# Kernel tuning notes

Hardware: AMD Instinct MI355X
Metric: run time of the kernel (lower is better)

## Reference

```python
import jax, jax.numpy as jnp
import numpy as np

NUM_CLASSES = 80
STRIDES = (8, 16, 32)
FEAT_HW = ((80, 80), (40, 40), (20, 20))
B = 32
MAX_GT = 60


def setup_inputs() -> dict:
    key = jax.random.key(0)
    ks = jax.random.split(key, 6)
    feats = {}
    for i, (s, (h, w)) in enumerate(zip(STRIDES, FEAT_HW)):
        feats[f"feat{s}"] = jax.random.normal(ks[i], (B, 5 + NUM_CLASSES, h, w), jnp.float32)
    u = jax.random.uniform(ks[3], (B, MAX_GT, 4), jnp.float32)
    # cx,cy in [0,640), w,h in [8,128): realistic pixel-space gt boxes for a 640x640 image
    gt_boxes = jnp.concatenate([u[..., :2] * 640.0, u[..., 2:] * 120.0 + 8.0], -1)
    gt_classes = jax.random.randint(ks[4], (B, MAX_GT), 0, NUM_CLASSES)
    num_gts = jax.random.randint(ks[5], (B,), 1, MAX_GT + 1)
    return dict(feat8=feats["feat8"], feat16=feats["feat16"], feat32=feats["feat32"],
                gt_boxes=gt_boxes, gt_classes=gt_classes, num_gts=num_gts)


def _decode(feat, stride):
    # torch get_output_and_grid: xy=(raw+grid)*stride, wh=exp(raw)*stride
    b, c, h, w = feat.shape
    yv, xv = jnp.meshgrid(jnp.arange(h), jnp.arange(w), indexing="ij")
    gx = xv.reshape(-1).astype(feat.dtype)  # [H*W]
    gy = yv.reshape(-1).astype(feat.dtype)
    out = feat.reshape(b, c, h * w).transpose(0, 2, 1)  # [B,A,C]
    xy = (out[..., :2] + jnp.stack([gx, gy], -1)[None]) * stride
    wh = jnp.exp(out[..., 2:4]) * stride
    return jnp.concatenate([xy, wh, out[..., 4:]], -1), gx, gy


def _pair_iou(a, b):
    # a: [G,4] xywh, b: [A,4] xywh -> [G,A] IoU (bboxes_iou, xyxy=False)
    tl = jnp.maximum(a[:, None, :2] - a[:, None, 2:] * 0.5, b[None, :, :2] - b[None, :, 2:] * 0.5)
    br = jnp.minimum(a[:, None, :2] + a[:, None, 2:] * 0.5, b[None, :, :2] + b[None, :, 2:] * 0.5)
    en = jnp.all(tl < br, -1)
    inter = jnp.where(en, jnp.prod(br - tl, -1), 0.0)
    area_a = jnp.prod(a[:, 2:], -1)
    area_b = jnp.prod(b[:, 2:], -1)
    return inter / (area_a[:, None] + area_b[None, :] - inter + 1e-16)


def _bce_logits(x, t):
    return jnp.maximum(x, 0.0) - x * t + jnp.log1p(jnp.exp(-jnp.abs(x)))


def _iou_loss(pred, tgt):
    # IOUloss(loss_type='iou'): 1 - iou^2, per box
    tl = jnp.maximum(pred[..., :2] - pred[..., 2:] * 0.5, tgt[..., :2] - tgt[..., 2:] * 0.5)
    br = jnp.minimum(pred[..., :2] + pred[..., 2:] * 0.5, tgt[..., :2] + tgt[..., 2:] * 0.5)
    en = jnp.all(tl < br, -1)
    inter = jnp.where(en, jnp.prod(br - tl, -1), 0.0)
    union = jnp.prod(pred[..., 2:], -1) + jnp.prod(tgt[..., 2:], -1) - inter
    iou = inter / (union + 1e-16)
    return 1.0 - iou ** 2


def _assign(boxes, cls_lo, obj_lo, gtb, gtc, vmask, cx, cy, st):
    # SimOTA per image. boxes [A,4], cls_lo [A,C], obj_lo [A], gtb [G,4], gtc [G] int,
    # vmask [G] bool (gt padding), cx/cy/st [A] anchor centers & strides.
    G, A = gtb.shape[0], boxes.shape[0]
    iou = _pair_iou(gtb, boxes)  # [G,A]
    gx, gy = gtb[:, :1], gtb[:, 1:2]
    gw, gh = gtb[:, 2:3], gtb[:, 3:4]
    in_box = ((cx[None] > gx - 0.5 * gw) & (cx[None] < gx + 0.5 * gw) &
              (cy[None] > gy - 0.5 * gh) & (cy[None] < gy + 0.5 * gh))
    R = 2.5  # center sampling radius (in strides)
    in_ctr = ((cx[None] > gx - R * st[None]) & (cx[None] < gx + R * st[None]) &
              (cy[None] > gy - R * st[None]) & (cy[None] < gy + R * st[None]))
    fg = ((in_box | in_ctr) & vmask[:, None]).any(0)  # [A] candidate anchors
    in_both = (in_box & in_ctr).astype(boxes.dtype)
    # pairwise cls cost: BCE(sqrt(sig(cls)*sig(obj)), onehot(gt_cls)).sum(-1),
    # decomposed to avoid the [G,A,C] tensor: sum_c bce0 + (bce1-bce0)[gt_cls]
    p = jnp.clip(jnp.sqrt(jax.nn.sigmoid(cls_lo) * jax.nn.sigmoid(obj_lo)[:, None]), 1e-7, 1.0 - 1e-7)
    bce1 = -jnp.log(p)          # [A,C]
    bce0 = -jnp.log(1.0 - p)    # [A,C]
    cls_cost = bce0.sum(-1)[None, :] + (bce1 - bce0)[:, gtc].T  # [G,A]
    cost = (cls_cost + 3.0 * (-jnp.log(iou + 1e-8))
            + 100000.0 * (1.0 - in_both)
            + 1e9 * (~fg)[None, :].astype(boxes.dtype)
            + 1e9 * (~vmask)[:, None].astype(boxes.dtype))
    K = 10  # n_candidate_k
    topk_ious, _ = jax.lax.top_k(iou * fg[None, :], K)
    dyn_k = jnp.maximum(topk_ious.sum(-1).astype(jnp.int32), 1)  # clamp(int(sum), min=1)
    _, pos = jax.lax.top_k(-cost, K)  # [G,K] lowest-cost anchors per gt
    sel = (jnp.arange(K)[None, :] < dyn_k[:, None]).astype(boxes.dtype)
    matching = jnp.zeros((G, A), boxes.dtype).at[jnp.arange(G)[:, None], pos].set(sel)
    matching = matching * vmask[:, None].astype(boxes.dtype)
    # resolve anchors claimed by >1 gt: keep min-cost gt
    conflict = matching.sum(0) > 1
    best_gt = jnp.argmin(cost, axis=0)  # [A]
    matching = jnp.where(conflict[None, :], jax.nn.one_hot(best_gt, G, dtype=matching.dtype).T, matching)
    fg_final = matching.sum(0) > 0  # [A]
    matched = jnp.argmax(matching, axis=0)  # [A]
    pred_iou = (matching * iou).sum(0)  # [A]
    cls_t = jax.nn.one_hot(gtc[matched], NUM_CLASSES, dtype=boxes.dtype) * pred_iou[:, None]
    reg_t = gtb[matched]
    return fg_final, cls_t, reg_t


def _forward(feat8, feat16, feat32, gt_boxes, gt_classes, num_gts):
    outs, cxs, cys, sts = [], [], [], []
    for f, s in zip((feat8, feat16, feat32), STRIDES):
        o, gx, gy = _decode(f, float(s))
        outs.append(o)
        cxs.append((gx + 0.5) * s)
        cys.append((gy + 0.5) * s)
        sts.append(jnp.full_like(gx, s))
    preds = jnp.concatenate(outs, 1)  # [B,A,5+C]
    cx = jnp.concatenate(cxs)
    cy = jnp.concatenate(cys)
    st = jnp.concatenate(sts)
    boxes = preds[..., :4]
    obj_lo = preds[..., 4]
    cls_lo = preds[..., 5:]
    vmask = jnp.arange(MAX_GT)[None, :] < num_gts[:, None]
    fg, cls_t, reg_t = jax.vmap(_assign, in_axes=(0, 0, 0, 0, 0, 0, None, None, None))(
        boxes, cls_lo, obj_lo, gt_boxes, gt_classes, vmask, cx, cy, st)
    # SimOTA assignment is no_grad in YOLOX: targets are constants wrt preds
    fg = jax.lax.stop_gradient(fg)
    cls_t = jax.lax.stop_gradient(cls_t)
    reg_t = jax.lax.stop_gradient(reg_t)
    fg_f = fg.astype(boxes.dtype)
    num_fg = jnp.maximum(fg_f.sum(), 1.0)
    loss_iou = (_iou_loss(boxes, reg_t) * fg_f).sum()
    loss_obj = _bce_logits(obj_lo, fg_f * 0.9).sum()  # obj_targets * 0.9 smoothing
    loss_cls = (_bce_logits(cls_lo, cls_t) * fg_f[..., None]).sum()
    REG_WEIGHT = 5.0
    return (REG_WEIGHT * loss_iou + loss_obj + loss_cls) / num_fg


def reference(feat8, feat16, feat32, gt_boxes, gt_classes, num_gts):
    return _forward(feat8, feat16, feat32, gt_boxes, gt_classes, num_gts)
```

## Files before the change

kernel.cpp:

```cpp
#include <hip/hip_runtime.h>

constexpr int kB = 32;
constexpr int kA = 8400;
constexpr int kG = 60;
constexpr int kC = 80;
constexpr int kK = 10;
constexpr int kNBx = (kA + 255)/256;
constexpr int kNB = kNBx * kB;

__device__ __forceinline__ float fexp(float x){ return __expf(x); }
__device__ __forceinline__ float flog(float x){ return __logf(x); }
__device__ __forceinline__ float frcp(float x){ return __builtin_amdgcn_rcpf(x); }
__device__ __forceinline__ float frsq(float x){ return __builtin_amdgcn_rsqf(x); }
__device__ __forceinline__ float fsqrt(float x){ return __builtin_amdgcn_sqrtf(x); }
__device__ __forceinline__ float fdiv(float a, float b){ return a * __builtin_amdgcn_rcpf(b); }
__device__ __forceinline__ float sigm(float x){ return frcp(1.0f + fexp(-x)); }
__device__ __forceinline__ float bce(float x, float t){
  return fmaxf(x, 0.0f) - x*t + flog(1.0f + fexp(-fabsf(x)));
}

__device__ __forceinline__ unsigned ordbits(float v){
  unsigned u = __float_as_uint(v);
  return (u & 0x80000000u) ? ~u : (u | 0x80000000u);
}
__device__ __forceinline__ float unpackf(unsigned k){
  return __uint_as_float((k & 0x80000000u) ? (k & 0x7fffffffu) : ~k);
}

struct AInfo { int x, y; float st; };
__device__ __forceinline__ AInfo ainfo(int a){
  AInfo r;
  if (a < 6400)      { r.x = a % 80;           r.y = a / 80;           r.st = 8.0f;  }
  else if (a < 8000) { int l = a-6400; r.x = l % 40; r.y = l / 40;     r.st = 16.0f; }
  else               { int l = a-8000; r.x = l % 20; r.y = l / 20;     r.st = 32.0f; }
  return r;
}

__device__ __forceinline__ float featv(const float* __restrict__ f8,
                                       const float* __restrict__ f16,
                                       const float* __restrict__ f32x,
                                       int b, int ch, int a){
  if (a < 6400) return f8 [(b*85 + ch)*6400 + a];
  if (a < 8000) return f16[(b*85 + ch)*1600 + (a - 6400)];
  return             f32x[(b*85 + ch)*400  + (a - 8000)];
}

__device__ __forceinline__ float pair_iou(float4 g, float4 p){
  float tlx = fmaxf(g.x - g.z*0.5f, p.x - p.z*0.5f);
  float tly = fmaxf(g.y - g.w*0.5f, p.y - p.w*0.5f);
  float brx = fminf(g.x + g.z*0.5f, p.x + p.z*0.5f);
  float bry = fminf(g.y + g.w*0.5f, p.y + p.w*0.5f);
  float inter = (tlx < brx && tly < bry) ? (brx-tlx)*(bry-tly) : 0.0f;
  return fdiv(inter, g.z*g.w + p.z*p.w - inter + 1e-16f);
}

__device__ __forceinline__ float cost_core(float iou, float cl, float obs, float b0sum,
                                           int a, float4 gt, int fg_a){
  AInfo ai = ainfo(a);
  float cx = ((float)ai.x + 0.5f)*ai.st;
  float cy = ((float)ai.y + 0.5f)*ai.st;
  bool in_box = (cx > gt.x - 0.5f*gt.z) && (cx < gt.x + 0.5f*gt.z)
             && (cy > gt.y - 0.5f*gt.w) && (cy < gt.y + 0.5f*gt.w);
  bool in_ctr = (cx > gt.x - 2.5f*ai.st) && (cx < gt.x + 2.5f*ai.st)
             && (cy > gt.y - 2.5f*ai.st) && (cy < gt.y + 2.5f*ai.st);
  float p = fsqrt(sigm(cl) * obs);
  p = fminf(fmaxf(p, 1e-7f), 1.0f - 1e-7f);
  float diff = -flog(p) + flog(1.0f - p);
  float c = b0sum + diff;
  c += 3.0f * (-flog(iou + 1e-8f));
  c += (in_box && in_ctr) ? 0.0f : 100000.0f;
  c += fg_a ? 0.0f : 1000000000.0f;
  return c;
}

__device__ __forceinline__ unsigned long long wave_max64(unsigned long long v){
  #pragma unroll
  for (int off = 32; off; off >>= 1){
    unsigned long long o = __shfl_xor(v, off, 64);
    if (o > v) v = o;
  }
  return v;
}

__global__ __launch_bounds__(256, 4) void k_decode(
    const float* __restrict__ f8, const float* __restrict__ f16, const float* __restrict__ f32x,
    const float* __restrict__ gtb, const int* __restrict__ ngts,
    float* __restrict__ boxes, float* __restrict__ boxesZ,
    float* __restrict__ objl, float* __restrict__ b0s,
    float* __restrict__ bceS, float* __restrict__ obsA,
    int* __restrict__ fg, int* __restrict__ cnt, int* __restrict__ mtch){
  int b = blockIdx.y;
  int tid = threadIdx.x;
  int a = blockIdx.x*256 + tid;
  __shared__ float4 sg[kG];
  if (tid < kG) sg[tid] = ((const float4*)gtb)[b*kG + tid];
  __syncthreads();
  if (a >= kA) return;
  int ng = ngts[b];
  const float* base; int hw, off; float st_; int gx, gy;
  if (a < 6400)      { base=f8;   hw=6400; off=a;        st_=8.0f;  gx=off%80; gy=off/80; }
  else if (a < 8000) { base=f16;  hw=1600; off=a-6400;   st_=16.0f; gx=off%40; gy=off/40; }
  else               { base=f32x; hw=400;  off=a-8000;   st_=32.0f; gx=off%20; gy=off/20; }
  const float* p0 = base + ((size_t)b*85)*hw + off;
  const float* pc = p0 + (size_t)5*hw;
  float t0 = p0[0];
  float t1 = p0[(size_t)hw];
  float t2 = p0[(size_t)2*hw];
  float t3 = p0[(size_t)3*hw];
  float ob = p0[(size_t)4*hw];
  float cl[kC];
  #pragma unroll
  for (int j = 0; j < kC; ++j) cl[j] = pc[(size_t)j*hw];
  __builtin_amdgcn_sched_barrier(0);
  float4 bx;
  bx.x = (t0 + (float)gx) * st_;
  bx.y = (t1 + (float)gy) * st_;
  bx.z = fexp(t2) * st_;
  bx.w = fexp(t3) * st_;
  int idx = b*kA + a;
  ((float4*)boxes)[idx] = bx;
  objl[idx] = ob;
  float obs = sigm(ob);
  obsA[idx] = obs;
  cnt[idx] = 0;
  mtch[idx] = 0x7fffffff;
  float cx = ((float)gx + 0.5f)*st_;
  float cy = ((float)gy + 0.5f)*st_;
  int f = 0;
  for (int g = 0; g < ng; ++g){
    float4 gt = sg[g];
    bool in_box = (cx > gt.x - 0.5f*gt.z) && (cx < gt.x + 0.5f*gt.z)
               && (cy > gt.y - 0.5f*gt.w) && (cy < gt.y + 0.5f*gt.w);
    bool in_ctr = (cx > gt.x - 2.5f*st_) && (cx < gt.x + 2.5f*st_)
               && (cy > gt.y - 2.5f*st_) && (cy < gt.y + 2.5f*st_);
    if (in_box || in_ctr){ f = 1; break; }
  }
  fg[idx] = f;
  ((float4*)boxesZ)[idx] = f ? bx : make_float4(0.0f,0.0f,0.0f,0.0f);
  float so = fsqrt(obs);
  float s = 0.0f;
  float sumCl = 0.0f;
  float slogv = 0.0f;
  #pragma unroll
  for (int grp = 0; grp < kC/8; ++grp){
    float prodS = 1.0f, prodV = 1.0f;
    #pragma unroll
    for (int j = 0; j < 8; ++j){
      float c = cl[grp*8 + j];
      float u = fexp(-c);
      float v = 1.0f + u;
      float p = so * frsq(v);
      p = fminf(fmaxf(p, 1e-7f), 1.0f - 1e-7f);
      prodS *= (1.0f - p);
      prodV *= v;
      sumCl += c;
    }
    s -= flog(prodS);
    slogv += flog(prodV);
  }
  b0s[idx] = s;
  bceS[idx] = sumCl + slogv;
}

__global__ __launch_bounds__(256) void k_assign(
    const float* __restrict__ f8, const float* __restrict__ f16, const float* __restrict__ f32x,
    const float* __restrict__ gtb, const int* __restrict__ gtc, const int* __restrict__ ngts,
    const float* __restrict__ boxes, const float* __restrict__ boxesZ,
    const float* __restrict__ obsA, const float* __restrict__ b0s,
    const int* __restrict__ fg,
    int* __restrict__ cnt, int* __restrict__ mtch){
  int b = blockIdx.x / kG;
  int g = blockIdx.x % kG;
  if (g >= ngts[b]) return;
  int tid = threadIdx.x;
  int lane = tid & 63, wid = tid >> 6;
  float4 gt = ((const float4*)gtb)[b*kG + g];
  int cls = gtc[b*kG + g];
  const float4* bx4 = (const float4*)boxes;
  const float4* bz4 = (const float4*)boxesZ;
  const float* c8  = f8   + ((size_t)b*85 + 5 + cls)*6400;
  const float* c16 = f16  + ((size_t)b*85 + 5 + cls)*1600;
  const float* c32 = f32x + ((size_t)b*85 + 5 + cls)*400;

  __shared__ unsigned long long lds_k[4*kK];
  __shared__ int lds_cnt[4];
  __shared__ int s_dynk;

  unsigned long long k1[kK];
  #pragma unroll
  for (int i = 0; i < kK; ++i) k1[i] = 0ull;

  for (int i = tid; i < kA; i += 256){
    float4 bx = bz4[b*kA + i];
    float v = pair_iou(gt, bx);
    unsigned long long key1 = ((unsigned long long)ordbits(v) << 32) | (unsigned)(~i);
    if (key1 > k1[kK-1]){
      k1[kK-1] = key1;
      #pragma unroll
      for (int i2 = kK-1; i2 > 0; --i2)
        if (k1[i2] > k1[i2-1]){ unsigned long long t = k1[i2]; k1[i2] = k1[i2-1]; k1[i2-1] = t; }
    }
  }
  {
    unsigned long long wtop = 0ull;
    #pragma unroll
    for (int k = 0; k < kK; ++k){
      unsigned long long best = wave_max64(k1[0]);
      if (k1[0] == best){
        #pragma unroll
        for (int i2 = 0; i2 < kK-1; ++i2) k1[i2] = k1[i2+1];
        k1[kK-1] = 0ull;
      }
      if (lane == k) wtop = best;
    }
    if (lane < kK) lds_k[wid*kK + lane] = wtop;
  }
  __syncthreads();
  if (wid == 0){
    unsigned long long key = (lane < 4*kK) ? lds_k[lane] : 0ull;
    float ksum = 0.0f;
    #pragma unroll
    for (int k = 0; k < kK; ++k){
      unsigned long long best = wave_max64(key);
      if (key == best) key = 0ull;
      if (best) ksum += unpackf((unsigned)(best >> 32));
    }
    if (lane == 0) s_dynk = max((int)ksum, 1);
  }
  __syncthreads();
  int dynk = s_dynk;

  int x00,y00,nx0,n0, x01,y01,nx1,n1, x02,y02,nx2,n2;
  {
    auto rect = [&](float st, int W, int& rx0, int& ry0, int& rnx, int& rn){
      float lox = fmaxf(gt.x - 0.5f*gt.z, gt.x - 2.5f*st);
      float hix = fminf(gt.x + 0.5f*gt.z, gt.x + 2.5f*st);
      float loy = fmaxf(gt.y - 0.5f*gt.w, gt.y - 2.5f*st);
      float hiy = fminf(gt.y + 0.5f*gt.w, gt.y + 2.5f*st);
      float rs = frcp(st);
      int ax0 = max(0,   (int)floorf(lox*rs - 0.5f) - 1);
      int ax1 = min(W-1, (int)ceilf (hix*rs - 0.5f) + 1);
      int ay0 = max(0,   (int)floorf(loy*rs - 0.5f) - 1);
      int ay1 = min(W-1, (int)ceilf (hiy*rs - 0.5f) + 1);
      rx0 = ax0; ry0 = ay0;
      rnx = max(0, ax1 - ax0 + 1);
      int rny = max(0, ay1 - ay0 + 1);
      rn = rnx * rny;
    };
    rect( 8.0f, 80, x00, y00, nx0, n0);
    rect(16.0f, 40, x01, y01, nx1, n1);
    rect(32.0f, 20, x02, y02, nx2, n2);
  }
  int total = n0 + n1 + n2;

  unsigned long long ck = 0ull;
  int nvalid = 0;
  if (tid < total){
    int i = tid, ix, iy, a; float st;
    if (i < n0)           { ix = x00 + i % nx0; iy = y00 + i / nx0; a = iy*80 + ix;          st = 8.0f;  }
    else if (i < n0 + n1) { int j = i - n0;      ix = x01 + j % nx1; iy = y01 + j / nx1; a = 6400 + iy*40 + ix; st = 16.0f; }
    else                  { int j = i - n0 - n1; ix = x02 + j % nx2; iy = y02 + j / nx2; a = 8000 + iy*20 + ix; st = 32.0f; }
    float cx = ((float)ix + 0.5f)*st;
    float cy = ((float)iy + 0.5f)*st;
    bool in_box = (cx > gt.x - 0.5f*gt.z) && (cx < gt.x + 0.5f*gt.z)
               && (cy > gt.y - 0.5f*gt.w) && (cy < gt.y + 0.5f*gt.w);
    bool in_ctr = (cx > gt.x - 2.5f*st) && (cx < gt.x + 2.5f*st)
               && (cy > gt.y - 2.5f*st) && (cy < gt.y + 2.5f*st);
    if (in_box && in_ctr){
      int idx = b*kA + a;
      float4 bx = bx4[idx];
      float iou = pair_iou(gt, bx);
      float cl = (a < 6400) ? c8[a] : (a < 8000) ? c16[a-6400] : c32[a-8000];
      float c = cost_core(iou, cl, obsA[idx], b0s[idx], a, gt, 1);
      ck = ~(((unsigned long long)ordbits(c) << 32) | (unsigned)a);
      nvalid = 1;
    }
  }
  {
    unsigned long long bal = __ballot(nvalid);
    if (lane == 0) lds_cnt[wid] = __popcll(bal);
    unsigned long long wtop = 0ull;
    #pragma unroll
    for (int k = 0; k < kK; ++k){
      unsigned long long best = wave_max64(ck);
      if (ck == best) ck = 0ull;
      if (lane == k) wtop = best;
    }
    if (lane < kK) lds_k[wid*kK + lane] = wtop;
  }
  __syncthreads();
  int cnt_total = lds_cnt[0] + lds_cnt[1] + lds_cnt[2] + lds_cnt[3];
  bool fb = (dynk > cnt_total);

  if (!fb){
    if (wid == 0){
      unsigned long long key = (lane < 4*kK) ? lds_k[lane] : 0ull;
      unsigned long long mine = 0ull;
      #pragma unroll
      for (int k = 0; k < kK; ++k){
        unsigned long long best = wave_max64(key);
        if (key == best) key = 0ull;
        if (lane == k) mine = best;
      }
      if (lane < dynk && mine){
        int a = (int)((unsigned)(~mine));
        atomicAdd(&cnt[b*kA + a], 1);
        atomicMin(&mtch[b*kA + a], g);
      }
    }
    return;
  }

  __syncthreads();
  unsigned long long k2[kK];
  #pragma unroll
  for (int i = 0; i < kK; ++i) k2[i] = 0ull;
  for (int i = tid; i < kA; i += 256){
    int idx = b*kA + i;
    float4 bx = bx4[idx];
    float iou = pair_iou(gt, bx);
    int fga = fg[idx];
    float cl = (i < 6400) ? c8[i] : (i < 8000) ? c16[i-6400] : c32[i-8000];
    float c = cost_core(iou, cl, obsA[idx], b0s[idx], i, gt, fga);
    unsigned long long key2 = ~(((unsigned long long)ordbits(c) << 32) | (unsigned)i);
    if (key2 > k2[kK-1]){
      k2[kK-1] = key2;
      #pragma unroll
      for (int i2 = kK-1; i2 > 0; --i2)
        if (k2[i2] > k2[i2-1]){ unsigned long long t = k2[i2]; k2[i2] = k2[i2-1]; k2[i2-1] = t; }
    }
  }
  {
    unsigned long long wtop = 0ull;
    #pragma unroll
    for (int k = 0; k < kK; ++k){
      unsigned long long best = wave_max64(k2[0]);
      if (k2[0] == best){
        #pragma unroll
        for (int i2 = 0; i2 < kK-1; ++i2) k2[i2] = k2[i2+1];
        k2[kK-1] = 0ull;
      }
      if (lane == k) wtop = best;
    }
    if (lane < kK) lds_k[wid*kK + lane] = wtop;
  }
  __syncthreads();
  if (wid == 0){
    unsigned long long key = (lane < 4*kK) ? lds_k[lane] : 0ull;
    unsigned long long mine = 0ull;
    #pragma unroll
    for (int k = 0; k < kK; ++k){
      unsigned long long best = wave_max64(key);
      if (key == best) key = 0ull;
      if (lane == k) mine = best;
    }
    if (lane < dynk && mine){
      int a = (int)((unsigned)(~mine));
      atomicAdd(&cnt[b*kA + a], 1);
      atomicMin(&mtch[b*kA + a], g);
    }
  }
}

__global__ __launch_bounds__(256) void k_loss(
    const float* __restrict__ f8, const float* __restrict__ f16, const float* __restrict__ f32x,
    const float* __restrict__ gtb, const int* __restrict__ gtc, const int* __restrict__ ngts,
    const float* __restrict__ boxes, const float* __restrict__ objl, const float* __restrict__ b0s,
    const float* __restrict__ bceS, const float* __restrict__ obsA,
    const int* __restrict__ fg, const int* __restrict__ cnt, const int* __restrict__ mtch,
    float4* __restrict__ pacc){
  int b = blockIdx.y;
  int a = blockIdx.x*256 + threadIdx.x;
  int tid = threadIdx.x;
  __shared__ float4 sg[kG];
  __shared__ int scls[kG];
  if (tid < kG){ sg[tid] = ((const float4*)gtb)[b*kG + tid]; scls[tid] = gtc[b*kG + tid]; }
  __syncthreads();
  float li = 0.0f, lo = 0.0f, lc = 0.0f, nf = 0.0f;
  bool valid = (a < kA);
  int idx = valid ? (b*kA + a) : (b*kA);
  int c = valid ? cnt[idx] : 0;
  float ob = valid ? objl[idx] : 0.0f;
  float4 bx = valid ? ((const float4*)boxes)[idx] : make_float4(0,0,1,1);

  float fgf = 0.0f; int mg = 0;
  if (valid && c == 1){ mg = mtch[idx]; fgf = 1.0f; }
  bool need = valid && (c > 1);
  if (__any(need)){
    if (need){
      int ng = ngts[b];
      float b0 = b0s[idx];
      float obs = obsA[idx];
      int fga = fg[idx];
      float bestc = 3.0e38f; int bg = 0;
      for (int g = 0; g < ng; ++g){
        float iou = pair_iou(sg[g], bx);
        float cl = featv(f8,f16,f32x,b,5+scls[g],a);
        float cst = cost_core(iou, cl, obs, b0, a, sg[g], fga);
        if (cst < bestc){ bestc = cst; bg = g; }
      }
      mg = bg; fgf = 1.0f;
    }
  }
  if (valid){
    lo = bce(ob, fgf*0.9f);
    if (fgf > 0.0f){
      nf = 1.0f;
      float4 r = sg[mg];
      float piou = pair_iou(r, bx);
      float tlx = fmaxf(bx.x - bx.z*0.5f, r.x - r.z*0.5f);
      float tly = fmaxf(bx.y - bx.w*0.5f, r.y - r.w*0.5f);
      float brx = fminf(bx.x + bx.z*0.5f, r.x + r.z*0.5f);
      float bry = fminf(bx.y + bx.w*0.5f, r.y + r.w*0.5f);
      float inter = (tlx < brx && tly < bry) ? (brx-tlx)*(bry-tly) : 0.0f;
      float un = bx.z*bx.w + r.z*r.w - inter;
      float iou = fdiv(inter, un + 1e-16f);
      li = 1.0f - iou*iou;
      int tc = scls[mg];
      float cl_tc = featv(f8,f16,f32x,b,5+tc,a);
      lc = bceS[idx] - piou * cl_tc;
    }
  }
  for (int off = 32; off > 0; off >>= 1){
    li += __shfl_down(li, off, 64);
    lo += __shfl_down(lo, off, 64);
    lc += __shfl_down(lc, off, 64);
    nf += __shfl_down(nf, off, 64);
  }
  __shared__ float4 wred[4];
  int wid = tid >> 6;
  if ((tid & 63) == 0) wred[wid] = make_float4(li, lo, lc, nf);
  __syncthreads();
  if (tid == 0){
    float4 t = wred[0];
    for (int w = 1; w < 4; ++w){
      float4 o = wred[w];
      t.x += o.x; t.y += o.y; t.z += o.z; t.w += o.w;
    }
    pacc[blockIdx.y * gridDim.x + blockIdx.x] = t;
  }
}

__global__ __launch_bounds__(256) void k_final(
    const float4* __restrict__ pacc, float* __restrict__ out){
  int tid = threadIdx.x;
  float li = 0.0f, lo = 0.0f, lc = 0.0f, nf = 0.0f;
  for (int i = tid; i < kNB; i += 256){
    float4 p = pacc[i];
    li += p.x; lo += p.y; lc += p.z; nf += p.w;
  }
  for (int off = 32; off > 0; off >>= 1){
    li += __shfl_down(li, off, 64);
    lo += __shfl_down(lo, off, 64);
    lc += __shfl_down(lc, off, 64);
    nf += __shfl_down(nf, off, 64);
  }
  __shared__ float4 wred[4];
  int wid = tid >> 6;
  if ((tid & 63) == 0) wred[wid] = make_float4(li, lo, lc, nf);
  __syncthreads();
  if (tid == 0){
    float4 t = wred[0];
    for (int w = 1; w < 4; ++w){
      float4 o = wred[w];
      t.x += o.x; t.y += o.y; t.z += o.z; t.w += o.w;
    }
    out[0] = (5.0f*t.x + t.y + t.z) * frcp(fmaxf(t.w, 1.0f));
  }
}

extern "C" void kernel_launch(void* const* d_in, const int* in_sizes, int n_in,
                              void* d_out, int out_size, void* d_ws, size_t ws_size,
                              hipStream_t stream) {
  (void)in_sizes; (void)n_in; (void)out_size; (void)ws_size;
  const float* f8   = (const float*)d_in[0];
  const float* f16  = (const float*)d_in[1];
  const float* f32x = (const float*)d_in[2];
  const float* gtb  = (const float*)d_in[3];
  const int*   gtc  = (const int*)d_in[4];
  const int*   ngts = (const int*)d_in[5];
  float* out = (float*)d_out;

  const size_t BA = (size_t)kB*kA;
  float* ws     = (float*)d_ws;
  float* boxes  = ws;
  float* boxesZ = boxes  + BA*4;
  float* objl   = boxesZ + BA*4;
  float* b0s    = objl   + BA;
  float* bceS   = b0s    + BA;
  float* obsA   = bceS   + BA;
  int*   fg     = (int*)(obsA + BA);
  int*   cnt    = fg  + BA;
  int*   mtch   = cnt + BA;
  float4* pacc  = (float4*)(mtch + BA);

  dim3 gBA(kNBx, kB);
  k_decode<<<gBA, dim3(256), 0, stream>>>(f8,f16,f32x,gtb,ngts,boxes,boxesZ,objl,b0s,bceS,obsA,fg,cnt,mtch);
  k_assign<<<dim3(kB*kG), dim3(256), 0, stream>>>(f8,f16,f32x,gtb,gtc,ngts,boxes,boxesZ,obsA,b0s,fg,cnt,mtch);
  k_loss<<<gBA, dim3(256), 0, stream>>>(f8,f16,f32x,gtb,gtc,ngts,boxes,objl,b0s,bceS,obsA,fg,cnt,mtch,pacc);
  k_final<<<dim3(1), dim3(256), 0, stream>>>(pacc, out);
}
```

Before: 203.4 us.

## Split decode class work across half-waves and fuse final reduction into loss kernel

The decode kernel now assigns two lanes per anchor, with each half-wave handling a different subset of the 80 class channels. The partial log-sums are combined through cross-lane shuffles, which raises parallelism and lowers per-thread register pressure (the 80-float class array is gone). The final reduction kernel is removed. The last loss block, detected with an atomic counter and threadfence, now does the global sum, which saves one launch. This adds a memset launch and an atomic last-block pattern, and the half-wave split is uneven (4 vs 6 groups).

```diff
diff --git a/kernel.cpp b/kernel.cpp
--- a/kernel.cpp
+++ b/kernel.cpp
@@ -7,6 +7,7 @@
 constexpr int kK = 10;
 constexpr int kNBx = (kA + 255)/256;
 constexpr int kNB = kNBx * kB;
+constexpr int kNDx = (kA + 127)/128;
 
 __device__ __forceinline__ float fexp(float x){ return __expf(x); }
 __device__ __forceinline__ float flog(float x){ return __logf(x); }
@@ -82,7 +83,7 @@
   return v;
 }
 
-__global__ __launch_bounds__(256, 4) void k_decode(
+__global__ __launch_bounds__(256) void k_decode(
     const float* __restrict__ f8, const float* __restrict__ f16, const float* __restrict__ f32x,
     const float* __restrict__ gtb, const int* __restrict__ ngts,
     float* __restrict__ boxes, float* __restrict__ boxesZ,
@@ -91,7 +92,10 @@
     int* __restrict__ fg, int* __restrict__ cnt, int* __restrict__ mtch){
   int b = blockIdx.y;
   int tid = threadIdx.x;
-  int a = blockIdx.x*256 + tid;
+  int wid = tid >> 6, lane = tid & 63;
+  int half = lane >> 5;
+  int l32 = lane & 31;
+  int a = blockIdx.x*128 + wid*32 + l32;
   __shared__ float4 sg[kG];
   if (tid < kG) sg[tid] = ((const float4*)gtb)[b*kG + tid];
   __syncthreads();
@@ -103,63 +107,85 @@
   else               { base=f32x; hw=400;  off=a-8000;   st_=32.0f; gx=off%20; gy=off/20; }
   const float* p0 = base + ((size_t)b*85)*hw + off;
   const float* pc = p0 + (size_t)5*hw;
-  float t0 = p0[0];
-  float t1 = p0[(size_t)hw];
-  float t2 = p0[(size_t)2*hw];
-  float t3 = p0[(size_t)3*hw];
+  int idx = b*kA + a;
+
   float ob = p0[(size_t)4*hw];
-  float cl[kC];
+  float obs = sigm(ob);
+  float so = fsqrt(obs);
+
+  int gbase = half ? 4 : 0;
+  int ngrp  = half ? 6 : 4;
+  float lS[6], lV[6];
+  float scl = 0.0f;
   #pragma unroll
-  for (int j = 0; j < kC; ++j) cl[j] = pc[(size_t)j*hw];
-  __builtin_amdgcn_sched_barrier(0);
-  float4 bx;
-  bx.x = (t0 + (float)gx) * st_;
-  bx.y = (t1 + (float)gy) * st_;
-  bx.z = fexp(t2) * st_;
-  bx.w = fexp(t3) * st_;
-  int idx = b*kA + a;
-  ((float4*)boxes)[idx] = bx;
-  objl[idx] = ob;
-  float obs = sigm(ob);
-  obsA[idx] = obs;
-  cnt[idx] = 0;
-  mtch[idx] = 0x7fffffff;
-  float cx = ((float)gx + 0.5f)*st_;
-  float cy = ((float)gy + 0.5f)*st_;
-  int f = 0;
-  for (int g = 0; g < ng; ++g){
-    float4 gt = sg[g];
-    bool in_box = (cx > gt.x - 0.5f*gt.z) && (cx < gt.x + 0.5f*gt.z)
-               && (cy > gt.y - 0.5f*gt.w) && (cy < gt.y + 0.5f*gt.w);
-    bool in_ctr = (cx > gt.x - 2.5f*st_) && (cx < gt.x + 2.5f*st_)
-               && (cy > gt.y - 2.5f*st_) && (cy < gt.y + 2.5f*st_);
-    if (in_box || in_ctr){ f = 1; break; }
-  }
-  fg[idx] = f;
-  ((float4*)boxesZ)[idx] = f ? bx : make_float4(0.0f,0.0f,0.0f,0.0f);
-  float so = fsqrt(obs);
-  float s = 0.0f;
-  float sumCl = 0.0f;
-  float slogv = 0.0f;
+  for (int gi = 0; gi < 6; ++gi){ lS[gi] = 0.0f; lV[gi] = 0.0f; }
   #pragma unroll
-  for (int grp = 0; grp < kC/8; ++grp){
-    float prodS = 1.0f, prodV = 1.0f;
+  for (int gi = 0; gi < 6; ++gi){
+    if (gi < ngrp){
+      int grp = gbase + gi;
+      float prodS = 1.0f, prodV = 1.0f;
+      #pragma unroll
+      for (int j = 0; j < 8; ++j){
+        float cv = pc[(size_t)(grp*8 + j)*hw];
+        float u = fexp(-cv);
+        float v = 1.0f + u;
+        float pp = so * frsq(v);
+        pp = fminf(fmaxf(pp, 1e-7f), 1.0f - 1e-7f);
+        prodS *= (1.0f - pp);
+        prodV *= v;
+        scl += cv;
+      }
+      lS[gi] = flog(prodS);
+      lV[gi] = flog(prodV);
+    }
+  }
+
+  if (half == 0){
+    float t0 = p0[0];
+    float t1 = p0[(size_t)hw];
+    float t2 = p0[(size_t)2*hw];
+    float t3 = p0[(size_t)3*hw];
+    float4 bx;
+    bx.x = (t0 + (float)gx) * st_;
+    bx.y = (t1 + (float)gy) * st_;
+    bx.z = fexp(t2) * st_;
+    bx.w = fexp(t3) * st_;
+    ((float4*)boxes)[idx] = bx;
+    objl[idx] = ob;
+    obsA[idx] = obs;
+    cnt[idx] = 0;
+    mtch[idx] = 0x7fffffff;
+    float cx = ((float)gx + 0.5f)*st_;
+    float cy = ((float)gy + 0.5f)*st_;
+    int f = 0;
+    for (int g = 0; g < ng; ++g){
+      float4 gt = sg[g];
+      bool in_box = (cx > gt.x - 0.5f*gt.z) && (cx < gt.x + 0.5f*gt.z)
+                 && (cy > gt.y - 0.5f*gt.w) && (cy < gt.y + 0.5f*gt.w);
+      bool in_ctr = (cx > gt.x - 2.5f*st_) && (cx < gt.x + 2.5f*st_)
+                 && (cy > gt.y - 2.5f*st_) && (cy < gt.y + 2.5f*st_);
+      if (in_box || in_ctr){ f = 1; break; }
+    }
+    fg[idx] = f;
+    ((float4*)boxesZ)[idx] = f ? bx : make_float4(0.0f,0.0f,0.0f,0.0f);
+  }
+
+  float s = 0.0f, slogv = 0.0f;
+  if (half == 0){
     #pragma unroll
-    for (int j = 0; j < 8; ++j){
-      float c = cl[grp*8 + j];
-      float u = fexp(-c);
-      float v = 1.0f + u;
-      float p = so * frsq(v);
-      p = fminf(fmaxf(p, 1e-7f), 1.0f - 1e-7f);
-      prodS *= (1.0f - p);
-      prodV *= v;
-      sumCl += c;
-    }
-    s -= flog(prodS);
-    slogv += flog(prodV);
-  }
-  b0s[idx] = s;
-  bceS[idx] = sumCl + slogv;
+    for (int gi = 0; gi < 4; ++gi){ s -= lS[gi]; slogv += lV[gi]; }
+  }
+  #pragma unroll
+  for (int gi = 0; gi < 6; ++gi){
+    float bs = __shfl(lS[gi], (lane + 32) & 63, 64);
+    float bv = __shfl(lV[gi], (lane + 32) & 63, 64);
+    if (half == 0){ s -= bs; slogv += bv; }
+  }
+  float sclB = __shfl(scl, (lane + 32) & 63, 64);
+  if (half == 0){
+    b0s[idx]  = s;
+    bceS[idx] = (scl + sclB) + slogv;
+  }
 }
 
 __global__ __launch_bounds__(256) void k_assign(
@@ -368,12 +394,13 @@
     const float* __restrict__ boxes, const float* __restrict__ objl, const float* __restrict__ b0s,
     const float* __restrict__ bceS, const float* __restrict__ obsA,
     const int* __restrict__ fg, const int* __restrict__ cnt, const int* __restrict__ mtch,
-    float4* __restrict__ pacc){
+    float4* __restrict__ pacc, int* __restrict__ done, float* __restrict__ out){
   int b = blockIdx.y;
   int a = blockIdx.x*256 + threadIdx.x;
   int tid = threadIdx.x;
   __shared__ float4 sg[kG];
   __shared__ int scls[kG];
+  __shared__ int slast;
   if (tid < kG){ sg[tid] = ((const float4*)gtb)[b*kG + tid]; scls[tid] = gtc[b*kG + tid]; }
   __syncthreads();
   float li = 0.0f, lo = 0.0f, lc = 0.0f, nf = 0.0f;
@@ -438,34 +465,35 @@
       t.x += o.x; t.y += o.y; t.z += o.z; t.w += o.w;
     }
     pacc[blockIdx.y * gridDim.x + blockIdx.x] = t;
-  }
-}
-
-__global__ __launch_bounds__(256) void k_final(
-    const float4* __restrict__ pacc, float* __restrict__ out){
-  int tid = threadIdx.x;
-  float li = 0.0f, lo = 0.0f, lc = 0.0f, nf = 0.0f;
-  for (int i = tid; i < kNB; i += 256){
-    float4 p = pacc[i];
-    li += p.x; lo += p.y; lc += p.z; nf += p.w;
-  }
-  for (int off = 32; off > 0; off >>= 1){
-    li += __shfl_down(li, off, 64);
-    lo += __shfl_down(lo, off, 64);
-    lc += __shfl_down(lc, off, 64);
-    nf += __shfl_down(nf, off, 64);
-  }
-  __shared__ float4 wred[4];
-  int wid = tid >> 6;
-  if ((tid & 63) == 0) wred[wid] = make_float4(li, lo, lc, nf);
-  __syncthreads();
-  if (tid == 0){
-    float4 t = wred[0];
-    for (int w = 1; w < 4; ++w){
-      float4 o = wred[w];
-      t.x += o.x; t.y += o.y; t.z += o.z; t.w += o.w;
-    }
-    out[0] = (5.0f*t.x + t.y + t.z) * frcp(fmaxf(t.w, 1.0f));
+    __threadfence();
+    int prev = atomicAdd(done, 1);
+    slast = (prev == kNB - 1) ? 1 : 0;
+  }
+  __syncthreads();
+  if (slast){
+    __threadfence();
+    float fi = 0.0f, fo = 0.0f, fc = 0.0f, fn = 0.0f;
+    const volatile float4* vp = (const volatile float4*)pacc;
+    for (int i = tid; i < kNB; i += 256){
+      float4 p; p.x = vp[i].x; p.y = vp[i].y; p.z = vp[i].z; p.w = vp[i].w;
+      fi += p.x; fo += p.y; fc += p.z; fn += p.w;
+    }
+    for (int off = 32; off > 0; off >>= 1){
+      fi += __shfl_down(fi, off, 64);
+      fo += __shfl_down(fo, off, 64);
+      fc += __shfl_down(fc, off, 64);
+      fn += __shfl_down(fn, off, 64);
+    }
+    if ((tid & 63) == 0) wred[wid] = make_float4(fi, fo, fc, fn);
+    __syncthreads();
+    if (tid == 0){
+      float4 t = wred[0];
+      for (int w = 1; w < 4; ++w){
+        float4 o = wred[w];
+        t.x += o.x; t.y += o.y; t.z += o.z; t.w += o.w;
+      }
+      out[0] = (5.0f*t.x + t.y + t.z) * frcp(fmaxf(t.w, 1.0f));
+    }
   }
 }
 
@@ -493,10 +521,12 @@
   int*   cnt    = fg  + BA;
   int*   mtch   = cnt + BA;
   float4* pacc  = (float4*)(mtch + BA);
-
+  int*   done   = (int*)(pacc + kNB);
+
+  hipMemsetAsync(done, 0, sizeof(int), stream);
+  dim3 gD(kNDx, kB);
+  k_decode<<<gD, dim3(256), 0, stream>>>(f8,f16,f32x,gtb,ngts,boxes,boxesZ,objl,b0s,bceS,obsA,fg,cnt,mtch);
+  k_assign<<<dim3(kB*kG), dim3(256), 0, stream>>>(f8,f16,f32x,gtb,gtc,ngts,boxes,boxesZ,obsA,b0s,fg,cnt,mtch);
   dim3 gBA(kNBx, kB);
-  k_decode<<<gBA, dim3(256), 0, stream>>>(f8,f16,f32x,gtb,ngts,boxes,boxesZ,objl,b0s,bceS,obsA,fg,cnt,mtch);
-  k_assign<<<dim3(kB*kG), dim3(256), 0, stream>>>(f8,f16,f32x,gtb,gtc,ngts,boxes,boxesZ,obsA,b0s,fg,cnt,mtch);
-  k_loss<<<gBA, dim3(256), 0, stream>>>(f8,f16,f32x,gtb,gtc,ngts,boxes,objl,b0s,bceS,obsA,fg,cnt,mtch,pacc);
-  k_final<<<dim3(1), dim3(256), 0, stream>>>(pacc, out);
-}
+  k_loss<<<gBA, dim3(256), 0, stream>>>(f8,f16,f32x,gtb,gtc,ngts,boxes,objl,b0s,bceS,obsA,fg,cnt,mtch,pacc,done,out);
+}
```

Result: slower. 223.1 us (+9.7%).

## Stream decode class logits through LDS with direct global-to-LDS pipelined loads

Applied to the files above, without the earlier changes.

The decode kernel used to load all 80 class logits into registers up front. It now uses global_load_lds to fill a 4-stage ring buffer in LDS, with manual vmcnt waits, so each group of 8 classes is computed while later groups are still in flight. Register pressure drops, and the occupancy hint in the launch bounds is removed. Out-of-range threads are clamped instead of returning early, so all lanes take part in the wave-level LDS loads, and all global stores move to the end. This adds 32KB of LDS per block, which may limit occupancy, and the hand-written waitcnt logic is fragile.

```diff
diff --git a/kernel.cpp b/kernel.cpp
--- a/kernel.cpp
+++ b/kernel.cpp
@@ -82,7 +82,20 @@
   return v;
 }
 
-__global__ __launch_bounds__(256, 4) void k_decode(
+__device__ __forceinline__ void stage1(const float* g, float* l){
+  __builtin_amdgcn_global_load_lds(
+      (const __attribute__((address_space(1))) void*)g,
+      (__attribute__((address_space(3))) void*)l, 4, 0, 0);
+}
+__device__ __forceinline__ void wait_vm(int n){
+  if      (n >= 24) asm volatile("s_waitcnt vmcnt(24)" ::: "memory");
+  else if (n >= 16) asm volatile("s_waitcnt vmcnt(16)" ::: "memory");
+  else if (n >= 8)  asm volatile("s_waitcnt vmcnt(8)"  ::: "memory");
+  else              asm volatile("s_waitcnt vmcnt(0)"  ::: "memory");
+  __builtin_amdgcn_sched_barrier(0);
+}
+
+__global__ __launch_bounds__(256) void k_decode(
     const float* __restrict__ f8, const float* __restrict__ f16, const float* __restrict__ f32x,
     const float* __restrict__ gtb, const int* __restrict__ ngts,
     float* __restrict__ boxes, float* __restrict__ boxesZ,
@@ -91,39 +104,43 @@
     int* __restrict__ fg, int* __restrict__ cnt, int* __restrict__ mtch){
   int b = blockIdx.y;
   int tid = threadIdx.x;
-  int a = blockIdx.x*256 + tid;
+  int a0 = blockIdx.x*256 + tid;
+  bool alive = (a0 < kA);
+  int a = alive ? a0 : (kA - 1);
   __shared__ float4 sg[kG];
+  __shared__ float buf[4][8][256];
   if (tid < kG) sg[tid] = ((const float4*)gtb)[b*kG + tid];
-  __syncthreads();
-  if (a >= kA) return;
   int ng = ngts[b];
+  __syncthreads();
+
   const float* base; int hw, off; float st_; int gx, gy;
   if (a < 6400)      { base=f8;   hw=6400; off=a;        st_=8.0f;  gx=off%80; gy=off/80; }
   else if (a < 8000) { base=f16;  hw=1600; off=a-6400;   st_=16.0f; gx=off%40; gy=off/40; }
   else               { base=f32x; hw=400;  off=a-8000;   st_=32.0f; gx=off%20; gy=off/20; }
   const float* p0 = base + ((size_t)b*85)*hw + off;
   const float* pc = p0 + (size_t)5*hw;
+  int wbase = (tid >> 6) * 64;
+
   float t0 = p0[0];
   float t1 = p0[(size_t)hw];
   float t2 = p0[(size_t)2*hw];
   float t3 = p0[(size_t)3*hw];
   float ob = p0[(size_t)4*hw];
-  float cl[kC];
+  __builtin_amdgcn_sched_barrier(0);
   #pragma unroll
-  for (int j = 0; j < kC; ++j) cl[j] = pc[(size_t)j*hw];
+  for (int g = 0; g < 4; ++g)
+    #pragma unroll
+    for (int j = 0; j < 8; ++j)
+      stage1(pc + (size_t)(g*8 + j)*hw, &buf[g][j][wbase]);
   __builtin_amdgcn_sched_barrier(0);
+
   float4 bx;
   bx.x = (t0 + (float)gx) * st_;
   bx.y = (t1 + (float)gy) * st_;
   bx.z = fexp(t2) * st_;
   bx.w = fexp(t3) * st_;
-  int idx = b*kA + a;
-  ((float4*)boxes)[idx] = bx;
-  objl[idx] = ob;
   float obs = sigm(ob);
-  obsA[idx] = obs;
-  cnt[idx] = 0;
-  mtch[idx] = 0x7fffffff;
+  float so = fsqrt(obs);
   float cx = ((float)gx + 0.5f)*st_;
   float cy = ((float)gy + 0.5f)*st_;
   int f = 0;
@@ -135,18 +152,27 @@
                && (cy > gt.y - 2.5f*st_) && (cy < gt.y + 2.5f*st_);
     if (in_box || in_ctr){ f = 1; break; }
   }
-  fg[idx] = f;
-  ((float4*)boxesZ)[idx] = f ? bx : make_float4(0.0f,0.0f,0.0f,0.0f);
-  float so = fsqrt(obs);
-  float s = 0.0f;
-  float sumCl = 0.0f;
-  float slogv = 0.0f;
+
+  float s = 0.0f, sumCl = 0.0f, slogv = 0.0f;
   #pragma unroll
-  for (int grp = 0; grp < kC/8; ++grp){
+  for (int g = 0; g < 10; ++g){
+    int rem = (9 - g < 3) ? (9 - g) : 3;
+    wait_vm(8 * rem);
+    float cv[8];
+    #pragma unroll
+    for (int j = 0; j < 8; ++j) cv[j] = buf[g & 3][j][tid];
+    asm volatile("s_waitcnt lgkmcnt(0)" ::: "memory");
+    __builtin_amdgcn_sched_barrier(0);
+    if (g + 4 < 10){
+      #pragma unroll
+      for (int j = 0; j < 8; ++j)
+        stage1(pc + (size_t)((g+4)*8 + j)*hw, &buf[g & 3][j][wbase]);
+    }
+    __builtin_amdgcn_sched_barrier(0);
     float prodS = 1.0f, prodV = 1.0f;
     #pragma unroll
     for (int j = 0; j < 8; ++j){
-      float c = cl[grp*8 + j];
+      float c = cv[j];
       float u = fexp(-c);
       float v = 1.0f + u;
       float p = so * frsq(v);
@@ -158,8 +184,19 @@
     s -= flog(prodS);
     slogv += flog(prodV);
   }
-  b0s[idx] = s;
-  bceS[idx] = sumCl + slogv;
+  __builtin_amdgcn_sched_barrier(0);
+  if (alive){
+    int idx = b*kA + a;
+    ((float4*)boxes)[idx] = bx;
+    objl[idx] = ob;
+    obsA[idx] = obs;
+    cnt[idx] = 0;
+    mtch[idx] = 0x7fffffff;
+    fg[idx] = f;
+    ((float4*)boxesZ)[idx] = f ? bx : make_float4(0.0f,0.0f,0.0f,0.0f);
+    b0s[idx]  = s;
+    bceS[idx] = sumCl + slogv;
+  }
 }
 
 __global__ __launch_bounds__(256) void k_assign(
```

Measured after the change: 198.7 us. -2.3%, faster.
